# Optimization experiments

Hardware: AMD Instinct MI355X
Metric: run time of the kernel (lower is better)

Reference implementation:

```python
import jax, jax.numpy as jnp
import numpy as np
import math

H = 12
DH = 64
MAX_POS = 1024

def setup_inputs() -> dict:
    key = jax.random.key(0)
    ks = jax.random.split(key, 8)
    B, L, D = 2, 1024, 768
    s = 0.02
    return {
        "hidden_states": jax.random.normal(ks[0], (B, L, D), jnp.float32),
        "attention_mask": jnp.zeros((B, 1, 1, L), jnp.float32),
        "struct_matrix": jax.random.uniform(ks[1], (5, B, 1, L, L), jnp.float32),
        "Wq": jax.random.normal(ks[2], (D, D), jnp.float32) * s,
        "bq": jnp.zeros((D,), jnp.float32),
        "Wk": jax.random.normal(ks[3], (D, D), jnp.float32) * s,
        "bk": jnp.zeros((D,), jnp.float32),
        "Wv": jax.random.normal(ks[4], (D, D), jnp.float32) * s,
        "bv": jnp.zeros((D,), jnp.float32),
        "dist_emb": jax.random.normal(ks[5], (2 * MAX_POS - 1, DH), jnp.float32) * s,
        "ssan_w": jax.random.normal(ks[6], (5, H, DH, DH), jnp.float32) * s,
        "abs_bias": jnp.zeros((5, H), jnp.float32),
    }

def reference(hidden_states, attention_mask, struct_matrix, Wq, bq, Wk, bk, Wv, bv, dist_emb, ssan_w, abs_bias):
    B, L, D = hidden_states.shape

    def heads(x):  # [B,L,D] -> [B,H,L,dh]
        return x.reshape(B, L, H, DH).transpose(0, 2, 1, 3)

    q = heads(hidden_states @ Wq + bq)
    k = heads(hidden_states @ Wk + bk)
    v = heads(hidden_states @ Wv + bv)

    scores = jnp.einsum('bhqd,bhkd->bhqk', q, k)

    # relative_key_query positional scores
    pos_ids = jnp.arange(L)
    distance = pos_ids[:, None] - pos_ids[None, :]          # [L,L]
    pos = dist_emb[distance + MAX_POS - 1]                  # [L,L,dh]
    scores = scores + jnp.einsum('bhld,lrd->bhlr', q, pos)
    scores = scores + jnp.einsum('bhrd,lrd->bhlr', k, pos)

    scores = scores / math.sqrt(DH)
    scores = scores + attention_mask

    # 5 SSAN bilinear bias terms, masked by structural matrices
    for i in range(5):
        bias = jnp.einsum('bhqd,hde,bhke->bhqk', q, ssan_w[i], k)
        scores = scores + (bias + abs_bias[i][None, :, None, None]) * struct_matrix[i]

    probs = jax.nn.softmax(scores, axis=-1)
    ctx = jnp.einsum('bhqk,bhkd->bqhd', probs, v).reshape(B, L, D)
    return ctx
```

## Files before the change

### kernel.cpp

```cpp
#include <hip/hip_runtime.h>
#include <math.h>

#define NB 2
#define NL 1024
#define ND 768
#define NH 12
#define DH 64

typedef _Float16 f16;
typedef _Float16 f16x2 __attribute__((ext_vector_type(2)));
typedef _Float16 f16x4 __attribute__((ext_vector_type(4)));
typedef _Float16 f16x8 __attribute__((ext_vector_type(8)));
typedef float f32x4 __attribute__((ext_vector_type(4)));

#define MFMA16(a, b, c) __builtin_amdgcn_mfma_f32_16x16x32_f16((a), (b), (c), 0, 0, 0)

__device__ __forceinline__ void soft_barrier() {
    asm volatile("s_waitcnt lgkmcnt(0)\n\ts_barrier" ::: "memory");
}

__global__ __launch_bounds__(256) void prep_kernel(
    const float* __restrict__ hs,
    const float* __restrict__ Wq, const float* __restrict__ Wk,
    const float* __restrict__ Wv, const float* __restrict__ sw,
    const float* __restrict__ de,
    f16* __restrict__ hsf, f16* __restrict__ wt, f16* __restrict__ swt,
    f16* __restrict__ de16)
{
    __shared__ float sT[64 * 66];
    const int t = threadIdx.x;
    const int tile = blockIdx.x;

    if (tile < 768) {
        const int base = tile * 2048 + t * 8;
        float4 a = *(const float4*)&hs[base];
        float4 b = *(const float4*)&hs[base + 4];
        f16x8 hv;
        hv[0] = (f16)a.x; hv[1] = (f16)a.y; hv[2] = (f16)a.z; hv[3] = (f16)a.w;
        hv[4] = (f16)b.x; hv[5] = (f16)b.y; hv[6] = (f16)b.z; hv[7] = (f16)b.w;
        *(f16x8*)&hsf[base] = hv;
        return;
    }
    if (tile >= 1260) {
        const int base = (tile - 1260) * 2048 + t * 8;
        if (base < 2047 * 64) {
            float4 a = *(const float4*)&de[base];
            float4 b = *(const float4*)&de[base + 4];
            f16x8 hv;
            hv[0] = (f16)a.x; hv[1] = (f16)a.y; hv[2] = (f16)a.z; hv[3] = (f16)a.w;
            hv[4] = (f16)b.x; hv[5] = (f16)b.y; hv[6] = (f16)b.z; hv[7] = (f16)b.w;
            *(f16x8*)&de16[base] = hv;
        }
        return;
    }

    const float* S; f16* D; int sRS, dRS;
    const int ti = tile - 768;
    if (ti < 432) {
        const int mat = ti / 144, r2 = ti % 144, ht = r2 / 12, kt = r2 % 12;
        const float* W = (mat == 0) ? Wq : (mat == 1) ? Wk : Wv;
        S = W + (size_t)(kt * 64) * ND + ht * 64;
        D = wt + (size_t)((mat * NH + ht) * 64) * ND + kt * 64;
        sRS = ND; dRS = ND;
    } else {
        const int i = ti - 432;
        S = sw + (size_t)i * 4096;
        D = swt + (size_t)i * 4096;
        sRS = 64; dRS = 64;
    }

    {
        const int kk = t >> 2, nb = (t & 3) * 16;
        float v[16];
        #pragma unroll
        for (int j = 0; j < 4; ++j)
            *(float4*)&v[4 * j] = *(const float4*)&S[(size_t)kk * sRS + nb + 4 * j];
        #pragma unroll
        for (int jj = 0; jj < 16; ++jj)
            sT[(nb + jj) * 66 + kk] = v[jj];
    }
    soft_barrier();
    {
        const int n = t >> 2, kb = (t & 3) * 16;
        f16 tmp[16];
        #pragma unroll
        for (int j = 0; j < 8; ++j) {
            float2 x = *(float2*)&sT[n * 66 + kb + 2 * j];
            tmp[2 * j]     = (f16)x.x;
            tmp[2 * j + 1] = (f16)x.y;
        }
        *(f16x8*)&D[(size_t)n * dRS + kb]     = *(f16x8*)&tmp[0];
        *(f16x8*)&D[(size_t)n * dRS + kb + 8] = *(f16x8*)&tmp[8];
    }
}

__global__ __launch_bounds__(256, 4) void qkv_kernel(
    const f16* __restrict__ hsf, const f16* __restrict__ wt,
    const float* __restrict__ bq, const float* __restrict__ bk,
    const float* __restrict__ bv,
    f16* __restrict__ qf, f16* __restrict__ kf, f16* __restrict__ vt)
{
    __shared__ f16 sA[64 * 72], sB[64 * 72];
    __shared__ float sT[64 * 66];

    const int m0  = blockIdx.x * 64;
    const int y   = blockIdx.y;
    const int mat = y / NH, h = y % NH;
    const int t = threadIdx.x, lane = t & 63, w = t >> 6;
    const int quad = lane >> 4, l15 = lane & 15;
    const int wm = w >> 1, wn = w & 1;

    const float* bias = (mat == 0) ? bq : (mat == 1) ? bk : bv;

    f32x4 acc[2][2];
    #pragma unroll
    for (int r = 0; r < 2; ++r)
        #pragma unroll
        for (int c = 0; c < 2; ++c) acc[r][c] = (f32x4){0.f, 0.f, 0.f, 0.f};

    const int srow = t >> 2, scol = (t & 3) * 16;
    const f16* Ag = hsf + (size_t)(m0 + srow) * ND + scol;
    const f16* Bg = wt + ((size_t)y * 64 + srow) * ND + scol;

    for (int k0 = 0; k0 < ND; k0 += 64) {
        soft_barrier();
        *(f16x8*)&sA[srow * 72 + scol]     = *(const f16x8*)&Ag[k0];
        *(f16x8*)&sA[srow * 72 + scol + 8] = *(const f16x8*)&Ag[k0 + 8];
        *(f16x8*)&sB[srow * 72 + scol]     = *(const f16x8*)&Bg[k0];
        *(f16x8*)&sB[srow * 72 + scol + 8] = *(const f16x8*)&Bg[k0 + 8];
        soft_barrier();
        #pragma unroll
        for (int kk = 0; kk < 64; kk += 32) {
            const int ko = kk + quad * 8;
            f16x8 a0 = *(f16x8*)&sA[(32 * wm + l15) * 72 + ko];
            f16x8 a1 = *(f16x8*)&sA[(32 * wm + 16 + l15) * 72 + ko];
            f16x8 b0 = *(f16x8*)&sB[(32 * wn + l15) * 72 + ko];
            f16x8 b1 = *(f16x8*)&sB[(32 * wn + 16 + l15) * 72 + ko];
            acc[0][0] = MFMA16(a0, b0, acc[0][0]);
            acc[0][1] = MFMA16(a0, b1, acc[0][1]);
            acc[1][0] = MFMA16(a1, b0, acc[1][0]);
            acc[1][1] = MFMA16(a1, b1, acc[1][1]);
        }
    }
    soft_barrier();

    const int bb = m0 >> 10;
    const int lbase = m0 & 1023;
    const int bh = bb * NH + h;

    if (mat < 2) {
        #pragma unroll
        for (int r = 0; r < 2; ++r)
            #pragma unroll
            for (int c = 0; c < 2; ++c) {
                const int col = 32 * wn + 16 * c + l15;
                const float bz = bias[h * 64 + col];
                #pragma unroll
                for (int rr = 0; rr < 4; ++rr)
                    sT[(32 * wm + 16 * r + 4 * quad + rr) * 66 + col] = acc[r][c][rr] + bz;
            }
        soft_barrier();
        const int orow = t >> 2, ocb = (t & 3) * 16;
        f16 tmp[16];
        #pragma unroll
        for (int j = 0; j < 8; ++j) {
            float2 x = *(float2*)&sT[orow * 66 + ocb + 2 * j];
            tmp[2 * j] = (f16)x.x; tmp[2 * j + 1] = (f16)x.y;
        }
        f16* dst = ((mat == 0) ? qf : kf) + ((size_t)bh * NL + lbase + orow) * DH + ocb;
        *(f16x8*)dst       = *(f16x8*)&tmp[0];
        *(f16x8*)(dst + 8) = *(f16x8*)&tmp[8];
    } else {
        #pragma unroll
        for (int r = 0; r < 2; ++r)
            #pragma unroll
            for (int c = 0; c < 2; ++c) {
                const int col = 32 * wn + 16 * c + l15;
                const float bz = bias[h * 64 + col];
                #pragma unroll
                for (int rr = 0; rr < 4; ++rr)
                    sT[col * 66 + 32 * wm + 16 * r + 4 * quad + rr] = acc[r][c][rr] + bz;
            }
        soft_barrier();
        const int d = t >> 2, lcb = (t & 3) * 16;
        f16 tmp[16];
        #pragma unroll
        for (int j = 0; j < 8; ++j) {
            float2 x = *(float2*)&sT[d * 66 + lcb + 2 * j];
            tmp[2 * j] = (f16)x.x; tmp[2 * j + 1] = (f16)x.y;
        }
        f16* dst = vt + ((size_t)bh * DH + d) * NL + lbase + lcb;
        *(f16x8*)dst       = *(f16x8*)&tmp[0];
        *(f16x8*)(dst + 8) = *(f16x8*)&tmp[8];
    }
}

__global__ __launch_bounds__(256, 4) void qw_kernel(
    const f16* __restrict__ qf, const f16* __restrict__ swt,
    f16* __restrict__ qwf)
{
    __shared__ f16 sA[64 * 72], sB[64 * 72];
    __shared__ float sT[64 * 66];

    const int l0 = blockIdx.x * 64;
    const int z  = blockIdx.y;
    const int p  = z / 24, bh = z % 24, h = bh % NH;
    const int t = threadIdx.x, lane = t & 63, w = t >> 6;
    const int quad = lane >> 4, l15 = lane & 15;
    const int wm = w >> 1, wn = w & 1;

    const int srow = t >> 2, scol = (t & 3) * 16;
    {
        const f16* As = qf + ((size_t)bh * NL + l0 + srow) * DH + scol;
        const f16* Bs = swt + ((size_t)(p * NH + h) * 64 + srow) * 64 + scol;
        *(f16x8*)&sA[srow * 72 + scol]     = *(const f16x8*)As;
        *(f16x8*)&sA[srow * 72 + scol + 8] = *(const f16x8*)(As + 8);
        *(f16x8*)&sB[srow * 72 + scol]     = *(const f16x8*)Bs;
        *(f16x8*)&sB[srow * 72 + scol + 8] = *(const f16x8*)(Bs + 8);
    }
    soft_barrier();

    f32x4 acc[2][2];
    #pragma unroll
    for (int r = 0; r < 2; ++r)
        #pragma unroll
        for (int c = 0; c < 2; ++c) acc[r][c] = (f32x4){0.f, 0.f, 0.f, 0.f};

    #pragma unroll
    for (int kk = 0; kk < 64; kk += 32) {
        const int ko = kk + quad * 8;
        f16x8 a0 = *(f16x8*)&sA[(32 * wm + l15) * 72 + ko];
        f16x8 a1 = *(f16x8*)&sA[(32 * wm + 16 + l15) * 72 + ko];
        f16x8 b0 = *(f16x8*)&sB[(32 * wn + l15) * 72 + ko];
        f16x8 b1 = *(f16x8*)&sB[(32 * wn + 16 + l15) * 72 + ko];
        acc[0][0] = MFMA16(a0, b0, acc[0][0]);
        acc[0][1] = MFMA16(a0, b1, acc[0][1]);
        acc[1][0] = MFMA16(a1, b0, acc[1][0]);
        acc[1][1] = MFMA16(a1, b1, acc[1][1]);
    }
    soft_barrier();

    #pragma unroll
    for (int r = 0; r < 2; ++r)
        #pragma unroll
        for (int c = 0; c < 2; ++c) {
            const int col = 32 * wn + 16 * c + l15;
            #pragma unroll
            for (int rr = 0; rr < 4; ++rr)
                sT[(32 * wm + 16 * r + 4 * quad + rr) * 66 + col] = acc[r][c][rr];
        }
    soft_barrier();

    const int orow = t >> 2, ocb = (t & 3) * 16;
    f16 tmp[16];
    #pragma unroll
    for (int j = 0; j < 8; ++j) {
        float2 x = *(float2*)&sT[orow * 66 + ocb + 2 * j];
        tmp[2 * j] = (f16)x.x; tmp[2 * j + 1] = (f16)x.y;
    }
    f16* dst = qwf + ((size_t)(p * 24 + bh) * NL + l0 + orow) * DH + ocb;
    *(f16x8*)dst       = *(f16x8*)&tmp[0];
    *(f16x8*)(dst + 8) = *(f16x8*)&tmp[8];
}

__global__ __launch_bounds__(256, 2) void attn_kernel(
    const f16* __restrict__ qf, const f16* __restrict__ kf,
    const f16* __restrict__ vt, const f16* __restrict__ qwf,
    const float* __restrict__ mask, const float* __restrict__ struct_m,
    const f16* __restrict__ de16, const float* __restrict__ abs_bias,
    float* __restrict__ out)
{
    __shared__ f16 sK[64 * 72];
    __shared__ f16 sVt[2][64 * 72];
    __shared__ f16 sE[96 * 72];
    __shared__ f16 sQEl[96 * 34];
    __shared__ f16 sKEl[96 * 34];
    __shared__ float sS[32 * 68];
    __shared__ f16 sP[32 * 72];
    __shared__ float sAlpha[32], sL[32];

    const int l0 = blockIdx.x * 32;
    const int bh = blockIdx.y;
    const int bb = bh / NH, h = bh % NH;
    const int t  = threadIdx.x;
    const int lane  = t & 63;
    const int w     = t >> 6;
    const int quad  = lane >> 4;
    const int l15   = lane & 15;
    const int msub  = w >> 1;
    const int npair = w & 1;

    const size_t NQKV = (size_t)NB * NH * NL * DH;

    f16x8 aQ[2], aW[5][2];
    {
        const size_t qrow = ((size_t)bh * NL + l0 + 16 * msub + l15) * DH;
        #pragma unroll
        for (int K = 0; K < 2; ++K) {
            aQ[K] = *(const f16x8*)&qf[qrow + 32 * K + 8 * quad];
            #pragma unroll
            for (int p = 0; p < 5; ++p)
                aW[p][K] = *(const f16x8*)&qwf[p * NQKV + qrow + 32 * K + 8 * quad];
        }
    }

    float ab[5];
    #pragma unroll
    for (int p = 0; p < 5; ++p) ab[p] = abs_bias[p * NH + h];

    float pf_st[5][2][4], pf_mask[2];

    auto stage_kv = [&](int r0s, int buf) {
        const int row = t >> 3, col = (t & 7) * 8;
        const f16* ks = kf + ((size_t)bh * NL + r0s) * DH;
        *(f16x8*)&sK[row * 72 + col]        = *(const f16x8*)&ks[row * 64 + col];
        *(f16x8*)&sK[(row + 32) * 72 + col] = *(const f16x8*)&ks[(row + 32) * 64 + col];
        const f16* vs = vt + (size_t)bh * DH * NL + r0s;
        *(f16x8*)&sVt[buf][row * 72 + col] =
            *(const f16x8*)&vs[(size_t)row * NL + col];
        *(f16x8*)&sVt[buf][(row + 32) * 72 + col] =
            *(const f16x8*)&vs[(size_t)(row + 32) * NL + col];
    };
    auto stage_E = [&](int r0s) {
        const int ebase = l0 - r0s + 960;
        #pragma unroll
        for (int p2 = 0; p2 < 3; ++p2) {
            const int idx = t + 256 * p2;
            const int er = idx >> 3, col = (idx & 7) * 8;
            if (er < 95)
                *(f16x8*)&sE[er * 72 + col] =
                    *(const f16x8*)&de16[(size_t)(ebase + er) * DH + col];
        }
    };
    auto prefetch = [&](int r0s) {
        #pragma unroll
        for (int n = 0; n < 2; ++n) {
            const int j = 32 * npair + 16 * n + l15;
            pf_mask[n] = mask[bb * NL + r0s + j];
            #pragma unroll
            for (int r = 0; r < 4; ++r) {
                const int i = 16 * msub + 4 * quad + r;
                #pragma unroll
                for (int p = 0; p < 5; ++p)
                    pf_st[p][n][r] =
                        struct_m[((size_t)(p * NB + bb) * NL + l0 + i) * NL + r0s + j];
            }
        }
    };

    stage_kv(0, 0);
    stage_E(0);
    prefetch(0);

    const int sm_i = t >> 3;
    const int sm_jb = t & 7;
    float m_cur = -INFINITY, l_cur = 0.f;
    f32x4 O[2];
    O[0] = (f32x4){0.f, 0.f, 0.f, 0.f};
    O[1] = (f32x4){0.f, 0.f, 0.f, 0.f};

    for (int kt = 0; kt < 16; ++kt) {
        const int cur = kt & 1;
        soft_barrier();

        {
            const int krow = (16 * w + l15) * 72;
            f16x8 ak0 = *(f16x8*)&sK[krow + quad * 8];
            f16x8 ak1 = *(f16x8*)&sK[krow + 32 + quad * 8];
            #pragma unroll
            for (int c = 0; c < 3; ++c) {
                const int nt = 3 - w + c;
                const int erow = (16 * nt + l15) * 72;
                f16x8 e0 = *(f16x8*)&sE[erow + quad * 8];
                f16x8 e1 = *(f16x8*)&sE[erow + 32 + quad * 8];
                f32x4 ck = (f32x4){0.f, 0.f, 0.f, 0.f};
                ck = MFMA16(ak0, e0, ck);
                ck = MFMA16(ak1, e1, ck);
                const int base = (16 * nt + l15) * 34 + 16 * w + 4 * quad;
                f16x2 lo = {(f16)ck[0], (f16)ck[1]};
                f16x2 hi = {(f16)ck[2], (f16)ck[3]};
                *(f16x2*)&sKEl[base]     = lo;
                *(f16x2*)&sKEl[base + 2] = hi;
            }
            const int qs = 3 * npair + msub;
            const int qc = 3 - npair;
            #pragma unroll
            for (int c = 0; c < 3; ++c) {
                if (c < qc) {
                    const int nt = qs + c;
                    const int erow = (16 * nt + l15) * 72;
                    f16x8 e0 = *(f16x8*)&sE[erow + quad * 8];
                    f16x8 e1 = *(f16x8*)&sE[erow + 32 + quad * 8];
                    f32x4 cq = (f32x4){0.f, 0.f, 0.f, 0.f};
                    cq = MFMA16(aQ[0], e0, cq);
                    cq = MFMA16(aQ[1], e1, cq);
                    const int base = (16 * nt + l15) * 34 + 16 * msub + 4 * quad;
                    f16x2 lo = {(f16)cq[0], (f16)cq[1]};
                    f16x2 hi = {(f16)cq[2], (f16)cq[3]};
                    *(f16x2*)&sQEl[base]     = lo;
                    *(f16x2*)&sQEl[base + 2] = hi;
                }
            }
        }
        soft_barrier();

        {
            f32x4 acc[2][6];
            #pragma unroll
            for (int n = 0; n < 2; ++n)
                #pragma unroll
                for (int p = 0; p < 6; ++p)
                    acc[n][p] = (f32x4){0.f, 0.f, 0.f, 0.f};

            #pragma unroll
            for (int K = 0; K < 2; ++K) {
                const int koff = K * 32 + quad * 8;
                f16x8 bk2[2];
                #pragma unroll
                for (int n = 0; n < 2; ++n)
                    bk2[n] = *(f16x8*)&sK[(32 * npair + 16 * n + l15) * 72 + koff];
                #pragma unroll
                for (int n = 0; n < 2; ++n)
                    acc[n][0] = MFMA16(aQ[K], bk2[n], acc[n][0]);
                #pragma unroll
                for (int p = 0; p < 5; ++p)
                    #pragma unroll
                    for (int n = 0; n < 2; ++n)
                        acc[n][1 + p] = MFMA16(aW[p][K], bk2[n], acc[n][1 + p]);
            }

            #pragma unroll
            for (int n = 0; n < 2; ++n) {
                const int j = 32 * npair + 16 * n + l15;
                #pragma unroll
                for (int r = 0; r < 4; ++r) {
                    const int i = 16 * msub + 4 * quad + r;
                    const int tp = i - j + 63;
                    float posv = (float)sQEl[tp * 34 + i] + (float)sKEl[tp * 34 + j];
                    float s = (acc[n][0][r] + posv) * 0.125f + pf_mask[n];
                    #pragma unroll
                    for (int p = 0; p < 5; ++p)
                        s += (acc[n][1 + p][r] + ab[p]) * pf_st[p][n][r];
                    sS[i * 68 + j] = s;
                }
            }
        }
        soft_barrier();

        {
            float sv[8];
            float smax = -INFINITY;
            #pragma unroll
            for (int k = 0; k < 8; ++k) {
                sv[k] = sS[sm_i * 68 + sm_jb + 8 * k];
                smax = fmaxf(smax, sv[k]);
            }
            #pragma unroll
            for (int off = 4; off > 0; off >>= 1)
                smax = fmaxf(smax, __shfl_xor(smax, off, 8));
            const float m_new = fmaxf(m_cur, smax);
            const float alpha = __expf(m_cur - m_new);
            float rsum = 0.f;
            #pragma unroll
            for (int k = 0; k < 8; ++k) {
                float p = __expf(sv[k] - m_new);
                sP[sm_i * 72 + sm_jb + 8 * k] = (f16)p;
                rsum += p;
            }
            #pragma unroll
            for (int off = 4; off > 0; off >>= 1)
                rsum += __shfl_xor(rsum, off, 8);
            l_cur = l_cur * alpha + rsum;
            m_cur = m_new;
            if (sm_jb == 0) { sAlpha[sm_i] = alpha; sL[sm_i] = l_cur; }
        }
        soft_barrier();

        {
            if (kt < 15) {
                stage_kv((kt + 1) * 64, cur ^ 1);
                stage_E((kt + 1) * 64);
                prefetch((kt + 1) * 64);
            }

            float a4[4];
            #pragma unroll
            for (int r = 0; r < 4; ++r) a4[r] = sAlpha[16 * msub + 4 * quad + r];
            #pragma unroll
            for (int n = 0; n < 2; ++n)
                #pragma unroll
                for (int r = 0; r < 4; ++r) O[n][r] *= a4[r];

            const int prow = (16 * msub + l15) * 72;
            #pragma unroll
            for (int K = 0; K < 2; ++K) {
                const int koff = K * 32 + quad * 8;
                f16x8 pfr = *(f16x8*)&sP[prow + koff];
                #pragma unroll
                for (int n = 0; n < 2; ++n) {
                    f16x8 vfr = *(f16x8*)&sVt[cur][(32 * npair + 16 * n + l15) * 72 + koff];
                    O[n] = MFMA16(pfr, vfr, O[n]);
                }
            }
        }
    }

    float linv[4];
    #pragma unroll
    for (int r = 0; r < 4; ++r) linv[r] = 1.0f / sL[16 * msub + 4 * quad + r];
    #pragma unroll
    for (int n = 0; n < 2; ++n) {
        const int dh = 32 * npair + 16 * n + l15;
        #pragma unroll
        for (int r = 0; r < 4; ++r) {
            const int i = 16 * msub + 4 * quad + r;
            out[((size_t)bb * NL + l0 + i) * ND + h * DH + dh] = O[n][r] * linv[r];
        }
    }
}

extern "C" void kernel_launch(void* const* d_in, const int* in_sizes, int n_in,
                              void* d_out, int out_size, void* d_ws, size_t ws_size,
                              hipStream_t stream) {
    const float* hs   = (const float*)d_in[0];
    const float* mask = (const float*)d_in[1];
    const float* stm  = (const float*)d_in[2];
    const float* Wq   = (const float*)d_in[3];
    const float* bq   = (const float*)d_in[4];
    const float* Wk   = (const float*)d_in[5];
    const float* bk   = (const float*)d_in[6];
    const float* Wv   = (const float*)d_in[7];
    const float* bv   = (const float*)d_in[8];
    const float* de   = (const float*)d_in[9];
    const float* sw   = (const float*)d_in[10];
    const float* abb  = (const float*)d_in[11];
    float* outp = (float*)d_out;

    const size_t NQKV = (size_t)NB * NH * NL * DH;
    char* ws = (char*)d_ws;
    f16* qf   = (f16*)ws;                 ws += NQKV * 2;
    f16* kf   = (f16*)ws;                 ws += NQKV * 2;
    f16* vtb  = (f16*)ws;                 ws += NQKV * 2;
    f16* qwf  = (f16*)ws;                 ws += 5 * NQKV * 2;
    f16* hsf  = (f16*)ws;                 ws += NQKV * 2;
    f16* wt   = (f16*)ws;                 ws += (size_t)2304 * 768 * 2;
    f16* swt  = (f16*)ws;                 ws += (size_t)245760 * 2;
    f16* de16 = (f16*)ws;

    prep_kernel<<<1324, 256, 0, stream>>>(hs, Wq, Wk, Wv, sw, de,
                                          hsf, wt, swt, de16);
    qkv_kernel<<<dim3(32, 36), 256, 0, stream>>>(hsf, wt, bq, bk, bv, qf, kf, vtb);
    qw_kernel<<<dim3(16, 120), 256, 0, stream>>>(qf, swt, qwf);
    attn_kernel<<<dim3(32, 24), 256, 0, stream>>>(qf, kf, vtb, qwf,
                                                  mask, stm, de16, abb, outp);
}
```

Measured before the change: 236.9 us.

## Keep softmax scores in registers, drop sS and V double buffer, raise occupancy

Scores now stay in MFMA accumulator registers. Row max and row sum are computed with cross-lane shuffles plus a small shared exchange between the two wave pairs, which removes the sS tile and the separate softmax pass. V is no longer double-buffered in LDS: the next tile is loaded into registers and written to LDS at the start of the next iteration, and launch bounds rise to 3 blocks per CU. s_setprio is placed around the MFMA sections. The goal is less LDS use and more resident waves, at the cost of more register pressure and one extra barrier per iteration for the reductions.

```diff
diff --git a/kernel.cpp b/kernel.cpp
--- a/kernel.cpp
+++ b/kernel.cpp
@@ -263,7 +263,7 @@
     *(f16x8*)(dst + 8) = *(f16x8*)&tmp[8];
 }
 
-__global__ __launch_bounds__(256, 2) void attn_kernel(
+__global__ __launch_bounds__(256, 3) void attn_kernel(
     const f16* __restrict__ qf, const f16* __restrict__ kf,
     const f16* __restrict__ vt, const f16* __restrict__ qwf,
     const float* __restrict__ mask, const float* __restrict__ struct_m,
@@ -271,13 +271,13 @@
     float* __restrict__ out)
 {
     __shared__ f16 sK[64 * 72];
-    __shared__ f16 sVt[2][64 * 72];
+    __shared__ f16 sVt[64 * 72];
     __shared__ f16 sE[96 * 72];
     __shared__ f16 sQEl[96 * 34];
     __shared__ f16 sKEl[96 * 34];
-    __shared__ float sS[32 * 68];
     __shared__ f16 sP[32 * 72];
-    __shared__ float sAlpha[32], sL[32];
+    __shared__ float sMax[64];
+    __shared__ float sSum[64];
 
     const int l0 = blockIdx.x * 32;
     const int bh = blockIdx.y;
@@ -309,17 +309,24 @@
     for (int p = 0; p < 5; ++p) ab[p] = abs_bias[p * NH + h];
 
     float pf_st[5][2][4], pf_mask[2];
-
-    auto stage_kv = [&](int r0s, int buf) {
+    f16x8 vreg[2];
+
+    auto stage_k = [&](int r0s) {
         const int row = t >> 3, col = (t & 7) * 8;
         const f16* ks = kf + ((size_t)bh * NL + r0s) * DH;
         *(f16x8*)&sK[row * 72 + col]        = *(const f16x8*)&ks[row * 64 + col];
         *(f16x8*)&sK[(row + 32) * 72 + col] = *(const f16x8*)&ks[(row + 32) * 64 + col];
+    };
+    auto load_v = [&](int r0s) {
+        const int row = t >> 3, col = (t & 7) * 8;
         const f16* vs = vt + (size_t)bh * DH * NL + r0s;
-        *(f16x8*)&sVt[buf][row * 72 + col] =
-            *(const f16x8*)&vs[(size_t)row * NL + col];
-        *(f16x8*)&sVt[buf][(row + 32) * 72 + col] =
-            *(const f16x8*)&vs[(size_t)(row + 32) * NL + col];
+        vreg[0] = *(const f16x8*)&vs[(size_t)row * NL + col];
+        vreg[1] = *(const f16x8*)&vs[(size_t)(row + 32) * NL + col];
+    };
+    auto write_v = [&]() {
+        const int row = t >> 3, col = (t & 7) * 8;
+        *(f16x8*)&sVt[row * 72 + col]        = vreg[0];
+        *(f16x8*)&sVt[(row + 32) * 72 + col] = vreg[1];
     };
     auto stage_E = [&](int r0s) {
         const int ebase = l0 - r0s + 960;
@@ -348,21 +355,22 @@
         }
     };
 
-    stage_kv(0, 0);
+    stage_k(0);
     stage_E(0);
+    load_v(0);
     prefetch(0);
 
-    const int sm_i = t >> 3;
-    const int sm_jb = t & 7;
-    float m_cur = -INFINITY, l_cur = 0.f;
+    float m_cur[4], l_cur[4];
+    #pragma unroll
+    for (int r = 0; r < 4; ++r) { m_cur[r] = -INFINITY; l_cur[r] = 0.f; }
     f32x4 O[2];
     O[0] = (f32x4){0.f, 0.f, 0.f, 0.f};
     O[1] = (f32x4){0.f, 0.f, 0.f, 0.f};
 
     for (int kt = 0; kt < 16; ++kt) {
-        const int cur = kt & 1;
-        soft_barrier();
-
+        soft_barrier();
+
+        write_v();
         {
             const int krow = (16 * w + l15) * 72;
             f16x8 ak0 = *(f16x8*)&sK[krow + quad * 8];
@@ -404,6 +412,7 @@
         }
         soft_barrier();
 
+        float sv[2][4];
         {
             f32x4 acc[2][6];
             #pragma unroll
@@ -412,6 +421,7 @@
                 for (int p = 0; p < 6; ++p)
                     acc[n][p] = (f32x4){0.f, 0.f, 0.f, 0.f};
 
+            __builtin_amdgcn_s_setprio(1);
             #pragma unroll
             for (int K = 0; K < 2; ++K) {
                 const int koff = K * 32 + quad * 8;
@@ -428,6 +438,7 @@
                     for (int n = 0; n < 2; ++n)
                         acc[n][1 + p] = MFMA16(aW[p][K], bk2[n], acc[n][1 + p]);
             }
+            __builtin_amdgcn_s_setprio(0);
 
             #pragma unroll
             for (int n = 0; n < 2; ++n) {
@@ -441,73 +452,94 @@
                     #pragma unroll
                     for (int p = 0; p < 5; ++p)
                         s += (acc[n][1 + p][r] + ab[p]) * pf_st[p][n][r];
-                    sS[i * 68 + j] = s;
+                    sv[n][r] = s;
                 }
             }
         }
-        soft_barrier();
-
         {
-            float sv[8];
-            float smax = -INFINITY;
-            #pragma unroll
-            for (int k = 0; k < 8; ++k) {
-                sv[k] = sS[sm_i * 68 + sm_jb + 8 * k];
-                smax = fmaxf(smax, sv[k]);
-            }
-            #pragma unroll
-            for (int off = 4; off > 0; off >>= 1)
-                smax = fmaxf(smax, __shfl_xor(smax, off, 8));
-            const float m_new = fmaxf(m_cur, smax);
-            const float alpha = __expf(m_cur - m_new);
-            float rsum = 0.f;
-            #pragma unroll
-            for (int k = 0; k < 8; ++k) {
-                float p = __expf(sv[k] - m_new);
-                sP[sm_i * 72 + sm_jb + 8 * k] = (f16)p;
-                rsum += p;
-            }
-            #pragma unroll
-            for (int off = 4; off > 0; off >>= 1)
-                rsum += __shfl_xor(rsum, off, 8);
-            l_cur = l_cur * alpha + rsum;
-            m_cur = m_new;
-            if (sm_jb == 0) { sAlpha[sm_i] = alpha; sL[sm_i] = l_cur; }
-        }
-        soft_barrier();
-
+            float pm[4];
+            #pragma unroll
+            for (int r = 0; r < 4; ++r) pm[r] = fmaxf(sv[0][r], sv[1][r]);
+            #pragma unroll
+            for (int off = 8; off > 0; off >>= 1)
+                #pragma unroll
+                for (int r = 0; r < 4; ++r)
+                    pm[r] = fmaxf(pm[r], __shfl_xor(pm[r], off));
+            if (l15 == 0) {
+                #pragma unroll
+                for (int r = 0; r < 4; ++r)
+                    sMax[npair * 32 + 16 * msub + 4 * quad + r] = pm[r];
+            }
+        }
+        soft_barrier();
+
+        float alpha[4];
         {
+            float ps[4];
+            #pragma unroll
+            for (int r = 0; r < 4; ++r) {
+                const int i = 16 * msub + 4 * quad + r;
+                const float m_t = fmaxf(sMax[i], sMax[32 + i]);
+                const float m_new = fmaxf(m_cur[r], m_t);
+                alpha[r] = __expf(m_cur[r] - m_new);
+                const float p0 = __expf(sv[0][r] - m_new);
+                const float p1 = __expf(sv[1][r] - m_new);
+                m_cur[r] = m_new;
+                sP[i * 72 + 32 * npair + l15]      = (f16)p0;
+                sP[i * 72 + 32 * npair + 16 + l15] = (f16)p1;
+                ps[r] = p0 + p1;
+            }
+            #pragma unroll
+            for (int off = 8; off > 0; off >>= 1)
+                #pragma unroll
+                for (int r = 0; r < 4; ++r)
+                    ps[r] += __shfl_xor(ps[r], off);
+            if (l15 == 0) {
+                #pragma unroll
+                for (int r = 0; r < 4; ++r)
+                    sSum[npair * 32 + 16 * msub + 4 * quad + r] = ps[r];
+            }
+        }
+        soft_barrier();
+
+        {
+            #pragma unroll
+            for (int r = 0; r < 4; ++r) {
+                const int i = 16 * msub + 4 * quad + r;
+                l_cur[r] = l_cur[r] * alpha[r] + sSum[i] + sSum[32 + i];
+            }
+
             if (kt < 15) {
-                stage_kv((kt + 1) * 64, cur ^ 1);
+                stage_k((kt + 1) * 64);
                 stage_E((kt + 1) * 64);
+                load_v((kt + 1) * 64);
                 prefetch((kt + 1) * 64);
             }
 
-            float a4[4];
-            #pragma unroll
-            for (int r = 0; r < 4; ++r) a4[r] = sAlpha[16 * msub + 4 * quad + r];
             #pragma unroll
             for (int n = 0; n < 2; ++n)
                 #pragma unroll
-                for (int r = 0; r < 4; ++r) O[n][r] *= a4[r];
+                for (int r = 0; r < 4; ++r) O[n][r] *= alpha[r];
 
             const int prow = (16 * msub + l15) * 72;
+            __builtin_amdgcn_s_setprio(1);
             #pragma unroll
             for (int K = 0; K < 2; ++K) {
                 const int koff = K * 32 + quad * 8;
                 f16x8 pfr = *(f16x8*)&sP[prow + koff];
                 #pragma unroll
                 for (int n = 0; n < 2; ++n) {
-                    f16x8 vfr = *(f16x8*)&sVt[cur][(32 * npair + 16 * n + l15) * 72 + koff];
+                    f16x8 vfr = *(f16x8*)&sVt[(32 * npair + 16 * n + l15) * 72 + koff];
                     O[n] = MFMA16(pfr, vfr, O[n]);
                 }
             }
+            __builtin_amdgcn_s_setprio(0);
         }
     }
 
     float linv[4];
     #pragma unroll
-    for (int r = 0; r < 4; ++r) linv[r] = 1.0f / sL[16 * msub + 4 * quad + r];
+    for (int r = 0; r < 4; ++r) linv[r] = 1.0f / l_cur[r];
     #pragma unroll
     for (int n = 0; n < 2; ++n) {
         const int dh = 32 * npair + 16 * n + l15;
```

After: 563.1 us. 138% more time.

## Fuse Q·W_ssan projection into attention kernel prologue

Applied to the files above, without the earlier changes.

Removes the separate qw_kernel that wrote five projected Q tensors to global memory. The attention kernel now computes Q·W_p per block with MFMA, staging results through the sE shared buffer, and loads them into registers. This drops a kernel launch and a large global write and read, at the cost of extra prologue MFMAs and barriers in each attention block.

```diff
diff --git a/kernel.cpp b/kernel.cpp
--- a/kernel.cpp
+++ b/kernel.cpp
@@ -195,77 +195,9 @@
     }
 }
 
-__global__ __launch_bounds__(256, 4) void qw_kernel(
-    const f16* __restrict__ qf, const f16* __restrict__ swt,
-    f16* __restrict__ qwf)
-{
-    __shared__ f16 sA[64 * 72], sB[64 * 72];
-    __shared__ float sT[64 * 66];
-
-    const int l0 = blockIdx.x * 64;
-    const int z  = blockIdx.y;
-    const int p  = z / 24, bh = z % 24, h = bh % NH;
-    const int t = threadIdx.x, lane = t & 63, w = t >> 6;
-    const int quad = lane >> 4, l15 = lane & 15;
-    const int wm = w >> 1, wn = w & 1;
-
-    const int srow = t >> 2, scol = (t & 3) * 16;
-    {
-        const f16* As = qf + ((size_t)bh * NL + l0 + srow) * DH + scol;
-        const f16* Bs = swt + ((size_t)(p * NH + h) * 64 + srow) * 64 + scol;
-        *(f16x8*)&sA[srow * 72 + scol]     = *(const f16x8*)As;
-        *(f16x8*)&sA[srow * 72 + scol + 8] = *(const f16x8*)(As + 8);
-        *(f16x8*)&sB[srow * 72 + scol]     = *(const f16x8*)Bs;
-        *(f16x8*)&sB[srow * 72 + scol + 8] = *(const f16x8*)(Bs + 8);
-    }
-    soft_barrier();
-
-    f32x4 acc[2][2];
-    #pragma unroll
-    for (int r = 0; r < 2; ++r)
-        #pragma unroll
-        for (int c = 0; c < 2; ++c) acc[r][c] = (f32x4){0.f, 0.f, 0.f, 0.f};
-
-    #pragma unroll
-    for (int kk = 0; kk < 64; kk += 32) {
-        const int ko = kk + quad * 8;
-        f16x8 a0 = *(f16x8*)&sA[(32 * wm + l15) * 72 + ko];
-        f16x8 a1 = *(f16x8*)&sA[(32 * wm + 16 + l15) * 72 + ko];
-        f16x8 b0 = *(f16x8*)&sB[(32 * wn + l15) * 72 + ko];
-        f16x8 b1 = *(f16x8*)&sB[(32 * wn + 16 + l15) * 72 + ko];
-        acc[0][0] = MFMA16(a0, b0, acc[0][0]);
-        acc[0][1] = MFMA16(a0, b1, acc[0][1]);
-        acc[1][0] = MFMA16(a1, b0, acc[1][0]);
-        acc[1][1] = MFMA16(a1, b1, acc[1][1]);
-    }
-    soft_barrier();
-
-    #pragma unroll
-    for (int r = 0; r < 2; ++r)
-        #pragma unroll
-        for (int c = 0; c < 2; ++c) {
-            const int col = 32 * wn + 16 * c + l15;
-            #pragma unroll
-            for (int rr = 0; rr < 4; ++rr)
-                sT[(32 * wm + 16 * r + 4 * quad + rr) * 66 + col] = acc[r][c][rr];
-        }
-    soft_barrier();
-
-    const int orow = t >> 2, ocb = (t & 3) * 16;
-    f16 tmp[16];
-    #pragma unroll
-    for (int j = 0; j < 8; ++j) {
-        float2 x = *(float2*)&sT[orow * 66 + ocb + 2 * j];
-        tmp[2 * j] = (f16)x.x; tmp[2 * j + 1] = (f16)x.y;
-    }
-    f16* dst = qwf + ((size_t)(p * 24 + bh) * NL + l0 + orow) * DH + ocb;
-    *(f16x8*)dst       = *(f16x8*)&tmp[0];
-    *(f16x8*)(dst + 8) = *(f16x8*)&tmp[8];
-}
-
 __global__ __launch_bounds__(256, 2) void attn_kernel(
     const f16* __restrict__ qf, const f16* __restrict__ kf,
-    const f16* __restrict__ vt, const f16* __restrict__ qwf,
+    const f16* __restrict__ vt, const f16* __restrict__ swt,
     const float* __restrict__ mask, const float* __restrict__ struct_m,
     const f16* __restrict__ de16, const float* __restrict__ abs_bias,
     float* __restrict__ out)
@@ -290,17 +222,50 @@
     const int msub  = w >> 1;
     const int npair = w & 1;
 
-    const size_t NQKV = (size_t)NB * NH * NL * DH;
-
     f16x8 aQ[2], aW[5][2];
     {
         const size_t qrow = ((size_t)bh * NL + l0 + 16 * msub + l15) * DH;
         #pragma unroll
-        for (int K = 0; K < 2; ++K) {
+        for (int K = 0; K < 2; ++K)
             aQ[K] = *(const f16x8*)&qf[qrow + 32 * K + 8 * quad];
-            #pragma unroll
-            for (int p = 0; p < 5; ++p)
-                aW[p][K] = *(const f16x8*)&qwf[p * NQKV + qrow + 32 * K + 8 * quad];
+    }
+
+    {
+        #pragma unroll
+        for (int b = 0; b < 2; ++b) {
+            const int pb0  = (b == 0) ? 0 : 3;
+            const int pcnt = (b == 0) ? 3 : 2;
+            #pragma unroll
+            for (int pi = 0; pi < 3; ++pi) {
+                if (pi < pcnt) {
+                    const int p = pb0 + pi;
+                    const f16* Wp = swt + ((size_t)(p * NH + h)) * 64 * 64;
+                    #pragma unroll
+                    for (int ntl = 0; ntl < 2; ++ntl) {
+                        const int nt = 2 * npair + ntl;
+                        f32x4 c = (f32x4){0.f, 0.f, 0.f, 0.f};
+                        #pragma unroll
+                        for (int K = 0; K < 2; ++K) {
+                            f16x8 bw = *(const f16x8*)&Wp[(size_t)(16 * nt + l15) * 64 + 32 * K + 8 * quad];
+                            c = MFMA16(aQ[K], bw, c);
+                        }
+                        #pragma unroll
+                        for (int r = 0; r < 4; ++r)
+                            sE[(pi * 32 + 16 * msub + 4 * quad + r) * 72 + 16 * nt + l15] = (f16)c[r];
+                    }
+                }
+            }
+            soft_barrier();
+            #pragma unroll
+            for (int pi = 0; pi < 3; ++pi) {
+                if (pi < pcnt) {
+                    #pragma unroll
+                    for (int K = 0; K < 2; ++K)
+                        aW[pb0 + pi][K] =
+                            *(const f16x8*)&sE[(pi * 32 + 16 * msub + l15) * 72 + 32 * K + 8 * quad];
+                }
+            }
+            soft_barrier();
         }
     }
 
@@ -541,7 +506,6 @@
     f16* qf   = (f16*)ws;                 ws += NQKV * 2;
     f16* kf   = (f16*)ws;                 ws += NQKV * 2;
     f16* vtb  = (f16*)ws;                 ws += NQKV * 2;
-    f16* qwf  = (f16*)ws;                 ws += 5 * NQKV * 2;
     f16* hsf  = (f16*)ws;                 ws += NQKV * 2;
     f16* wt   = (f16*)ws;                 ws += (size_t)2304 * 768 * 2;
     f16* swt  = (f16*)ws;                 ws += (size_t)245760 * 2;
@@ -550,7 +514,6 @@
     prep_kernel<<<1324, 256, 0, stream>>>(hs, Wq, Wk, Wv, sw, de,
                                           hsf, wt, swt, de16);
     qkv_kernel<<<dim3(32, 36), 256, 0, stream>>>(hsf, wt, bq, bk, bv, qf, kf, vtb);
-    qw_kernel<<<dim3(16, 120), 256, 0, stream>>>(qf, swt, qwf);
-    attn_kernel<<<dim3(32, 24), 256, 0, stream>>>(qf, kf, vtb, qwf,
+    attn_kernel<<<dim3(32, 24), 256, 0, stream>>>(qf, kf, vtb, swt,
                                                   mask, stm, de16, abb, outp);
 }
```

New measurement: 230.9 us. 1.03x faster.
